# Kernel tuning notes

Measured on AMD Instinct MI355X. Metric: run time of the kernel, lower is better.

Reference implementation:

```python
import jax, jax.numpy as jnp
import numpy as np

N_NODES = 100000
N_EDGES = 1600000
D_IN = 64
D_OUT = 64


def setup_inputs() -> dict:
    key = jax.random.key(0)
    k1, k2, k3, k4 = jax.random.split(key, 4)
    x = jax.random.normal(k1, (N_NODES, D_IN), dtype=jnp.float32)
    edge_index = jax.random.randint(k2, (2, N_EDGES), 0, N_NODES, dtype=jnp.int64)
    W = jax.random.normal(k3, (D_OUT, D_IN), dtype=jnp.float32) * (1.0 / np.sqrt(D_IN))
    b = jax.random.normal(k4, (D_OUT,), dtype=jnp.float32) * 0.01
    return {"x": x, "edge_index": edge_index, "W": W, "b": b}


def reference(x, edge_index, W, b):
    num_nodes = x.shape[0]
    row, col = edge_index[0], edge_index[1]
    # degree of each node as a destination (scatter_add of ones over row)
    deg = jax.ops.segment_sum(jnp.ones(row.shape[0], dtype=x.dtype), row,
                              num_segments=num_nodes)
    # deg^-0.5 with inf (deg==0) replaced by 0
    deg_inv_sqrt = jnp.where(deg > 0, jax.lax.rsqrt(jnp.maximum(deg, 1.0)) * jnp.where(deg > 0, 1.0, 0.0), 0.0)
    deg_inv_sqrt = jnp.where(deg > 0, deg ** -0.5, 0.0)
    # gather source features, scale by source norm, scatter-add to destinations
    weighted = x[col] * deg_inv_sqrt[col][:, None]          # [E, D_IN]
    agg = jax.ops.segment_sum(weighted, row, num_segments=num_nodes)  # [N, D_IN]
    agg = agg * deg_inv_sqrt[:, None]
    # linear + relu (torch Linear: y = agg @ W.T + b)
    return jax.nn.relu(agg @ W.T + b)
```

## Files before the change

### kernel.cpp

```cpp
#include <hip/hip_runtime.h>

#define N_NODES 100000
#define N_EDGES 1600000
#define NE4 400000
#define D 64

#define CSHIFT 7
#define CNODES 128
#define NCB 782
#define CAPC 2560
#define COLBITS 17
#define COLMASK 0x1FFFF

#define EPB 16384
#define SBLKS 98
#define XBLKS 1563

#define CCUR_OFF   0
#define CPAIRS_OFF 3200
#define RS_OFF     8010880
#define DINV_OFF   8412288
#define Y_OFF      8813696

typedef float fvec4 __attribute__((ext_vector_type(4)));
typedef __attribute__((ext_vector_type(8))) short bf16x8;
typedef __attribute__((ext_vector_type(4))) float f32x4;

__device__ __forceinline__ float bf2f(unsigned short u) {
    return __uint_as_float(((unsigned)u) << 16);
}
__device__ __forceinline__ unsigned f2bf(float f) {
    unsigned bits = __float_as_uint(f);
    return (bits + 0x7FFFu + ((bits >> 16) & 1u)) >> 16;
}

__global__ __launch_bounds__(256) void fat_kernel(
        const float* __restrict__ x, const float* __restrict__ W,
        const int* __restrict__ row, const int* __restrict__ col,
        int* __restrict__ ccur, int* __restrict__ cpairs,
        unsigned short* __restrict__ y) {
    __shared__ int lcnt[NCB];
    __shared__ int lbase[NCB];
    int t = threadIdx.x;
    if (blockIdx.x < SBLKS) {
        const int4* r4 = (const int4*)row;
        const int4* c4 = (const int4*)col;
        int base4 = blockIdx.x * (EPB / 4);
        for (int i = t; i < NCB; i += 256) lcnt[i] = 0;
        __syncthreads();
#pragma unroll
        for (int i = 0; i < EPB / 1024; ++i) {
            int i4 = base4 + i * 256 + t;
            if (i4 < NE4) {
                int4 rv = r4[i4];
                atomicAdd(&lcnt[rv.x >> CSHIFT], 1);
                atomicAdd(&lcnt[rv.y >> CSHIFT], 1);
                atomicAdd(&lcnt[rv.z >> CSHIFT], 1);
                atomicAdd(&lcnt[rv.w >> CSHIFT], 1);
            }
        }
        __syncthreads();
        for (int i = t; i < NCB; i += 256) {
            int cc = lcnt[i];
            lbase[i] = cc ? atomicAdd(&ccur[i], cc) : 0;
            lcnt[i] = 0;
        }
        __syncthreads();
#pragma unroll
        for (int i = 0; i < EPB / 1024; ++i) {
            int i4 = base4 + i * 256 + t;
            if (i4 < NE4) {
                int4 rv = r4[i4];
                int4 cv = c4[i4];
                int b0 = rv.x >> CSHIFT, b1 = rv.y >> CSHIFT;
                int b2 = rv.z >> CSHIFT, b3 = rv.w >> CSHIFT;
                int p0 = lbase[b0] + atomicAdd(&lcnt[b0], 1);
                int p1 = lbase[b1] + atomicAdd(&lcnt[b1], 1);
                int p2 = lbase[b2] + atomicAdd(&lcnt[b2], 1);
                int p3 = lbase[b3] + atomicAdd(&lcnt[b3], 1);
                if (p0 < CAPC) cpairs[(size_t)b0 * CAPC + p0] = ((rv.x & (CNODES - 1)) << COLBITS) | cv.x;
                if (p1 < CAPC) cpairs[(size_t)b1 * CAPC + p1] = ((rv.y & (CNODES - 1)) << COLBITS) | cv.y;
                if (p2 < CAPC) cpairs[(size_t)b2 * CAPC + p2] = ((rv.z & (CNODES - 1)) << COLBITS) | cv.z;
                if (p3 < CAPC) cpairs[(size_t)b3 * CAPC + p3] = ((rv.w & (CNODES - 1)) << COLBITS) | cv.w;
            }
        }
        return;
    }
    int wave = t >> 6, lane = t & 63;
    int n0w = (blockIdx.x - SBLKS) * 64 + wave * 16;
    if (n0w >= N_NODES) return;
    int lm = lane & 15;
    int g  = lane >> 4;
    bf16x8 ahi[2], alo[2];
    const float* xr = x + (size_t)(n0w + lm) * D + g * 8;
#pragma unroll
    for (int ks = 0; ks < 2; ++ks) {
        float4 fa = *(const float4*)(xr + ks * 32);
        float4 fb = *(const float4*)(xr + ks * 32 + 4);
        float f[8] = {fa.x, fa.y, fa.z, fa.w, fb.x, fb.y, fb.z, fb.w};
#pragma unroll
        for (int j = 0; j < 8; ++j) {
            unsigned hb = f2bf(f[j]);
            float r = f[j] - bf2f((unsigned short)hb);
            ahi[ks][j] = (short)hb;
            alo[ks][j] = (short)f2bf(r);
        }
    }
#pragma unroll
    for (int jt = 0; jt < 4; ++jt) {
        const float* wr = W + (size_t)(jt * 16 + lm) * D + g * 8;
        bf16x8 whi[2], wlo[2];
#pragma unroll
        for (int ks = 0; ks < 2; ++ks) {
            float4 fa = *(const float4*)(wr + ks * 32);
            float4 fb = *(const float4*)(wr + ks * 32 + 4);
            float f[8] = {fa.x, fa.y, fa.z, fa.w, fb.x, fb.y, fb.z, fb.w};
#pragma unroll
            for (int j = 0; j < 8; ++j) {
                unsigned hb = f2bf(f[j]);
                float r = f[j] - bf2f((unsigned short)hb);
                whi[ks][j] = (short)hb;
                wlo[ks][j] = (short)f2bf(r);
            }
        }
        f32x4 acc = {0.0f, 0.0f, 0.0f, 0.0f};
#pragma unroll
        for (int ks = 0; ks < 2; ++ks) {
            acc = __builtin_amdgcn_mfma_f32_16x16x32_bf16(ahi[ks], whi[ks], acc, 0, 0, 0);
            acc = __builtin_amdgcn_mfma_f32_16x16x32_bf16(alo[ks], whi[ks], acc, 0, 0, 0);
            acc = __builtin_amdgcn_mfma_f32_16x16x32_bf16(ahi[ks], wlo[ks], acc, 0, 0, 0);
        }
#pragma unroll
        for (int r = 0; r < 4; ++r) {
            int n = n0w + g * 4 + r;
            y[(size_t)n * D + jt * 16 + lm] = (unsigned short)f2bf(acc[r]);
        }
    }
}

__global__ __launch_bounds__(256) void hist_kernel(
        const int* __restrict__ ccur, const int* __restrict__ cpairs,
        int* __restrict__ rs, float* __restrict__ dinv) {
    __shared__ int hist[CNODES];
    __shared__ int sc[CNODES];
    int t = threadIdx.x;
    int cb = blockIdx.x;
    int base = cb * CAPC;
    int cnt = ccur[cb]; if (cnt > CAPC) cnt = CAPC;
    if (t < CNODES) hist[t] = 0;
    __syncthreads();
    for (int i = t; i < cnt; i += 256)
        atomicAdd(&hist[cpairs[base + i] >> COLBITS], 1);
    __syncthreads();
    int hv = (t < CNODES) ? hist[t] : 0;
    if (t < CNODES) sc[t] = hv;
    __syncthreads();
    for (int off = 1; off < CNODES; off <<= 1) {
        int u = (t < CNODES && t >= off) ? sc[t - off] : 0;
        __syncthreads();
        if (t < CNODES) sc[t] += u;
        __syncthreads();
    }
    if (t < CNODES) {
        int n = (cb << CSHIFT) + t;
        if (n < N_NODES) {
            rs[n] = base + sc[t] - hv;
            dinv[n] = (hv > 0) ? rsqrtf((float)hv) : 0.0f;
        }
    }
}

__global__ __launch_bounds__(512, 4) void megab_kernel(
        const int* __restrict__ ccur, const int* __restrict__ cpairs,
        const int* __restrict__ rs, const float* __restrict__ dinv,
        const unsigned short* __restrict__ y,
        const float* __restrict__ bias, float* __restrict__ out) {
    __shared__ int scol[CAPC];
    __shared__ int cur[CNODES];
    __shared__ int sst[CNODES + 1];
    int t = threadIdx.x;
    int cb = blockIdx.x;
    int base = cb * CAPC;
    int cnt = ccur[cb]; if (cnt > CAPC) cnt = CAPC;
    if (t < CNODES) {
        int n = (cb << CSHIFT) + t;
        int v = (n < N_NODES) ? rs[n] - base : cnt;
        cur[t] = v;
        sst[t] = v;
    }
    if (t == 0) sst[CNODES] = cnt;
    __syncthreads();
    for (int i = t; i < cnt; i += 512) {
        int p = cpairs[base + i];
        int pos = atomicAdd(&cur[p >> COLBITS], 1);
        scol[pos] = p & COLMASK;
    }
    __syncthreads();
    int wave = t >> 6, lane = t & 63;
    int g = lane >> 3, q = lane & 7;
    float bj[8];
    {
        float4 b0 = *(const float4*)(bias + q * 8);
        float4 b1 = *(const float4*)(bias + q * 8 + 4);
        bj[0] = b0.x; bj[1] = b0.y; bj[2] = b0.z; bj[3] = b0.w;
        bj[4] = b1.x; bj[5] = b1.y; bj[6] = b1.z; bj[7] = b1.w;
    }
#pragma unroll 1
    for (int pass = 0; pass < 2; ++pass) {
        int ln = pass * 64 + wave * 8 + g;
        int n = (cb << CSHIFT) + ln;
        int s = sst[ln], d = sst[ln + 1] - s;
        float a[8];
#pragma unroll
        for (int j = 0; j < 8; ++j) a[j] = 0.0f;
        int c8[8];
#pragma unroll
        for (int u = 0; u < 8; ++u) c8[u] = (u < d) ? scol[s + u] : 0;
        for (int k = 0; k < d; k += 8) {
            uint4 v[8];
            float dv8[8];
#pragma unroll
            for (int u = 0; u < 8; ++u) {
                if (k + u < d) {
                    int c = c8[u];
                    dv8[u] = dinv[c];
                    v[u] = *(const uint4*)(y + (size_t)c * D + q * 8);
                }
            }
#pragma unroll
            for (int u = 0; u < 8; ++u) {
                int e2 = k + 8 + u;
                c8[u] = (e2 < d) ? scol[s + e2] : 0;
            }
#pragma unroll
            for (int u = 0; u < 8; ++u) {
                if (k + u < d) {
                    float dvu = dv8[u];
                    a[0] = fmaf(dvu, __uint_as_float(v[u].x << 16),         a[0]);
                    a[1] = fmaf(dvu, __uint_as_float(v[u].x & 0xffff0000u), a[1]);
                    a[2] = fmaf(dvu, __uint_as_float(v[u].y << 16),         a[2]);
                    a[3] = fmaf(dvu, __uint_as_float(v[u].y & 0xffff0000u), a[3]);
                    a[4] = fmaf(dvu, __uint_as_float(v[u].z << 16),         a[4]);
                    a[5] = fmaf(dvu, __uint_as_float(v[u].z & 0xffff0000u), a[5]);
                    a[6] = fmaf(dvu, __uint_as_float(v[u].w << 16),         a[6]);
                    a[7] = fmaf(dvu, __uint_as_float(v[u].w & 0xffff0000u), a[7]);
                }
            }
        }
        if (n < N_NODES) {
            float dvn = dinv[n];
            fvec4 r0, r1;
            r0.x = fmaxf(fmaf(dvn, a[0], bj[0]), 0.0f);
            r0.y = fmaxf(fmaf(dvn, a[1], bj[1]), 0.0f);
            r0.z = fmaxf(fmaf(dvn, a[2], bj[2]), 0.0f);
            r0.w = fmaxf(fmaf(dvn, a[3], bj[3]), 0.0f);
            r1.x = fmaxf(fmaf(dvn, a[4], bj[4]), 0.0f);
            r1.y = fmaxf(fmaf(dvn, a[5], bj[5]), 0.0f);
            r1.z = fmaxf(fmaf(dvn, a[6], bj[6]), 0.0f);
            r1.w = fmaxf(fmaf(dvn, a[7], bj[7]), 0.0f);
            __builtin_nontemporal_store(r0, (fvec4*)(out + (size_t)n * D + q * 8));
            __builtin_nontemporal_store(r1, (fvec4*)(out + (size_t)n * D + q * 8 + 4));
        }
    }
}

extern "C" void kernel_launch(void* const* d_in, const int* in_sizes, int n_in,
                              void* d_out, int out_size, void* d_ws, size_t ws_size,
                              hipStream_t stream) {
    const float* x    = (const float*)d_in[0];
    const int*   eidx = (const int*)d_in[1];
    const float* W    = (const float*)d_in[2];
    const float* b    = (const float*)d_in[3];
    float* out = (float*)d_out;
    char* ws = (char*)d_ws;

    const int* row = eidx;
    const int* col = eidx + N_EDGES;

    int* ccur   = (int*)(ws + CCUR_OFF);
    int* cpairs = (int*)(ws + CPAIRS_OFF);
    int* rs     = (int*)(ws + RS_OFF);
    float* dinv = (float*)(ws + DINV_OFF);
    unsigned short* y = (unsigned short*)(ws + Y_OFF);

    hipMemsetAsync(ccur, 0, NCB * sizeof(int), stream);
    fat_kernel<<<SBLKS + XBLKS, 256, 0, stream>>>(x, W, row, col, ccur, cpairs, y);
    hist_kernel<<<NCB, 256, 0, stream>>>(ccur, cpairs, rs, dinv);
    megab_kernel<<<NCB, 512, 0, stream>>>(ccur, cpairs, rs, dinv, y, b, out);
}
```

Before: 161.1 us.

## Fuse memset, scatter, hist and gather into one cooperative persistent kernel

```diff
diff --git a/kernel.cpp b/kernel.cpp
--- a/kernel.cpp
+++ b/kernel.cpp
@@ -1,4 +1,7 @@
 #include <hip/hip_runtime.h>
+#include <hip/hip_cooperative_groups.h>
+
+namespace cg = cooperative_groups;
 
 #define N_NODES 100000
 #define N_EDGES 1600000
@@ -12,9 +15,9 @@
 #define COLBITS 17
 #define COLMASK 0x1FFFF
 
-#define EPB 16384
-#define SBLKS 98
-#define XBLKS 1563
+#define EPB 8192
+#define SBLKS 196
+#define GRID 512
 
 #define CCUR_OFF   0
 #define CPAIRS_OFF 3200
@@ -34,65 +37,64 @@
     return (bits + 0x7FFFu + ((bits >> 16) & 1u)) >> 16;
 }
 
-__global__ __launch_bounds__(256) void fat_kernel(
-        const float* __restrict__ x, const float* __restrict__ W,
+
+__device__ __forceinline__ void dev_scatter(int sb, int t,
         const int* __restrict__ row, const int* __restrict__ col,
         int* __restrict__ ccur, int* __restrict__ cpairs,
+        int* lcnt, int* lbase) {
+    const int4* r4 = (const int4*)row;
+    const int4* c4 = (const int4*)col;
+    int base4 = sb * (EPB / 4);
+    for (int i = t; i < NCB; i += 512) lcnt[i] = 0;
+    __syncthreads();
+#pragma unroll
+    for (int i = 0; i < EPB / 2048; ++i) {
+        int i4 = base4 + i * 512 + t;
+        if (i4 < NE4) {
+            int4 rv = r4[i4];
+            atomicAdd(&lcnt[rv.x >> CSHIFT], 1);
+            atomicAdd(&lcnt[rv.y >> CSHIFT], 1);
+            atomicAdd(&lcnt[rv.z >> CSHIFT], 1);
+            atomicAdd(&lcnt[rv.w >> CSHIFT], 1);
+        }
+    }
+    __syncthreads();
+    for (int i = t; i < NCB; i += 512) {
+        int cc = lcnt[i];
+        lbase[i] = cc ? atomicAdd(&ccur[i], cc) : 0;
+        lcnt[i] = 0;
+    }
+    __syncthreads();
+#pragma unroll
+    for (int i = 0; i < EPB / 2048; ++i) {
+        int i4 = base4 + i * 512 + t;
+        if (i4 < NE4) {
+            int4 rv = r4[i4];
+            int4 cv = c4[i4];
+            int b0 = rv.x >> CSHIFT, b1 = rv.y >> CSHIFT;
+            int b2 = rv.z >> CSHIFT, b3 = rv.w >> CSHIFT;
+            int p0 = lbase[b0] + atomicAdd(&lcnt[b0], 1);
+            int p1 = lbase[b1] + atomicAdd(&lcnt[b1], 1);
+            int p2 = lbase[b2] + atomicAdd(&lcnt[b2], 1);
+            int p3 = lbase[b3] + atomicAdd(&lcnt[b3], 1);
+            if (p0 < CAPC) cpairs[(size_t)b0 * CAPC + p0] = ((rv.x & (CNODES - 1)) << COLBITS) | cv.x;
+            if (p1 < CAPC) cpairs[(size_t)b1 * CAPC + p1] = ((rv.y & (CNODES - 1)) << COLBITS) | cv.y;
+            if (p2 < CAPC) cpairs[(size_t)b2 * CAPC + p2] = ((rv.z & (CNODES - 1)) << COLBITS) | cv.z;
+            if (p3 < CAPC) cpairs[(size_t)b3 * CAPC + p3] = ((rv.w & (CNODES - 1)) << COLBITS) | cv.w;
+        }
+    }
+}
+
+__device__ __forceinline__ void dev_xform(int u, int t,
+        const float* __restrict__ x, const float* __restrict__ W,
         unsigned short* __restrict__ y) {
-    __shared__ int lcnt[NCB];
-    __shared__ int lbase[NCB];
-    int t = threadIdx.x;
-    if (blockIdx.x < SBLKS) {
-        const int4* r4 = (const int4*)row;
-        const int4* c4 = (const int4*)col;
-        int base4 = blockIdx.x * (EPB / 4);
-        for (int i = t; i < NCB; i += 256) lcnt[i] = 0;
-        __syncthreads();
-#pragma unroll
-        for (int i = 0; i < EPB / 1024; ++i) {
-            int i4 = base4 + i * 256 + t;
-            if (i4 < NE4) {
-                int4 rv = r4[i4];
-                atomicAdd(&lcnt[rv.x >> CSHIFT], 1);
-                atomicAdd(&lcnt[rv.y >> CSHIFT], 1);
-                atomicAdd(&lcnt[rv.z >> CSHIFT], 1);
-                atomicAdd(&lcnt[rv.w >> CSHIFT], 1);
-            }
-        }
-        __syncthreads();
-        for (int i = t; i < NCB; i += 256) {
-            int cc = lcnt[i];
-            lbase[i] = cc ? atomicAdd(&ccur[i], cc) : 0;
-            lcnt[i] = 0;
-        }
-        __syncthreads();
-#pragma unroll
-        for (int i = 0; i < EPB / 1024; ++i) {
-            int i4 = base4 + i * 256 + t;
-            if (i4 < NE4) {
-                int4 rv = r4[i4];
-                int4 cv = c4[i4];
-                int b0 = rv.x >> CSHIFT, b1 = rv.y >> CSHIFT;
-                int b2 = rv.z >> CSHIFT, b3 = rv.w >> CSHIFT;
-                int p0 = lbase[b0] + atomicAdd(&lcnt[b0], 1);
-                int p1 = lbase[b1] + atomicAdd(&lcnt[b1], 1);
-                int p2 = lbase[b2] + atomicAdd(&lcnt[b2], 1);
-                int p3 = lbase[b3] + atomicAdd(&lcnt[b3], 1);
-                if (p0 < CAPC) cpairs[(size_t)b0 * CAPC + p0] = ((rv.x & (CNODES - 1)) << COLBITS) | cv.x;
-                if (p1 < CAPC) cpairs[(size_t)b1 * CAPC + p1] = ((rv.y & (CNODES - 1)) << COLBITS) | cv.y;
-                if (p2 < CAPC) cpairs[(size_t)b2 * CAPC + p2] = ((rv.z & (CNODES - 1)) << COLBITS) | cv.z;
-                if (p3 < CAPC) cpairs[(size_t)b3 * CAPC + p3] = ((rv.w & (CNODES - 1)) << COLBITS) | cv.w;
-            }
-        }
-        return;
-    }
     int wave = t >> 6, lane = t & 63;
-    int n0w = (blockIdx.x - SBLKS) * 64 + wave * 16;
+    int n0w = u * 128 + wave * 16;
     if (n0w >= N_NODES) return;
     int lm = lane & 15;
-    int g  = lane >> 4;
+    int gg = lane >> 4;
     bf16x8 ahi[2], alo[2];
-    const float* xr = x + (size_t)(n0w + lm) * D + g * 8;
+    const float* xr = x + (size_t)(n0w + lm) * D + gg * 8;
 #pragma unroll
     for (int ks = 0; ks < 2; ++ks) {
         float4 fa = *(const float4*)(xr + ks * 32);
@@ -108,7 +110,7 @@
     }
 #pragma unroll
     for (int jt = 0; jt < 4; ++jt) {
-        const float* wr = W + (size_t)(jt * 16 + lm) * D + g * 8;
+        const float* wr = W + (size_t)(jt * 16 + lm) * D + gg * 8;
         bf16x8 whi[2], wlo[2];
 #pragma unroll
         for (int ks = 0; ks < 2; ++ks) {
@@ -132,24 +134,22 @@
         }
 #pragma unroll
         for (int r = 0; r < 4; ++r) {
-            int n = n0w + g * 4 + r;
+            int n = n0w + gg * 4 + r;
             y[(size_t)n * D + jt * 16 + lm] = (unsigned short)f2bf(acc[r]);
         }
     }
 }
 
-__global__ __launch_bounds__(256) void hist_kernel(
+__device__ __forceinline__ void dev_hist(int b, int t,
         const int* __restrict__ ccur, const int* __restrict__ cpairs,
-        int* __restrict__ rs, float* __restrict__ dinv) {
-    __shared__ int hist[CNODES];
-    __shared__ int sc[CNODES];
-    int t = threadIdx.x;
-    int cb = blockIdx.x;
-    int base = cb * CAPC;
-    int cnt = ccur[cb]; if (cnt > CAPC) cnt = CAPC;
+        int* __restrict__ rs, float* __restrict__ dinv,
+        int* hist, int* sc) {
+    __syncthreads();
+    int base = b * CAPC;
+    int cnt = ccur[b]; if (cnt > CAPC) cnt = CAPC;
     if (t < CNODES) hist[t] = 0;
     __syncthreads();
-    for (int i = t; i < cnt; i += 256)
+    for (int i = t; i < cnt; i += 512)
         atomicAdd(&hist[cpairs[base + i] >> COLBITS], 1);
     __syncthreads();
     int hv = (t < CNODES) ? hist[t] : 0;
@@ -162,7 +162,7 @@
         __syncthreads();
     }
     if (t < CNODES) {
-        int n = (cb << CSHIFT) + t;
+        int n = (b << CSHIFT) + t;
         if (n < N_NODES) {
             rs[n] = base + sc[t] - hv;
             dinv[n] = (hv > 0) ? rsqrtf((float)hv) : 0.0f;
@@ -170,20 +170,17 @@
     }
 }
 
-__global__ __launch_bounds__(512, 4) void megab_kernel(
+__device__ __forceinline__ void dev_gather(int b, int t,
         const int* __restrict__ ccur, const int* __restrict__ cpairs,
         const int* __restrict__ rs, const float* __restrict__ dinv,
         const unsigned short* __restrict__ y,
-        const float* __restrict__ bias, float* __restrict__ out) {
-    __shared__ int scol[CAPC];
-    __shared__ int cur[CNODES];
-    __shared__ int sst[CNODES + 1];
-    int t = threadIdx.x;
-    int cb = blockIdx.x;
-    int base = cb * CAPC;
-    int cnt = ccur[cb]; if (cnt > CAPC) cnt = CAPC;
+        const float* __restrict__ bias, float* __restrict__ out,
+        int* scol, int* cur, int* sst) {
+    __syncthreads();
+    int base = b * CAPC;
+    int cnt = ccur[b]; if (cnt > CAPC) cnt = CAPC;
     if (t < CNODES) {
-        int n = (cb << CSHIFT) + t;
+        int n = (b << CSHIFT) + t;
         int v = (n < N_NODES) ? rs[n] - base : cnt;
         cur[t] = v;
         sst[t] = v;
@@ -208,7 +205,7 @@
 #pragma unroll 1
     for (int pass = 0; pass < 2; ++pass) {
         int ln = pass * 64 + wave * 8 + g;
-        int n = (cb << CSHIFT) + ln;
+        int n = (b << CSHIFT) + ln;
         int s = sst[ln], d = sst[ln + 1] - s;
         float a[8];
 #pragma unroll
@@ -264,13 +261,83 @@
     }
 }
 
+__global__ __launch_bounds__(512, 4) void gcn_kernel(
+        const float* __restrict__ x, const float* __restrict__ W,
+        const int* __restrict__ row, const int* __restrict__ col,
+        int* __restrict__ ccur, int* __restrict__ cpairs,
+        int* __restrict__ rs, float* __restrict__ dinv,
+        unsigned short* __restrict__ y,
+        const float* __restrict__ bias, float* __restrict__ out) {
+    cg::grid_group grid = cg::this_grid();
+    __shared__ int lcnt[NCB];
+    __shared__ int lbase[NCB];
+    __shared__ int hist[CNODES];
+    __shared__ int sc[CNODES];
+    __shared__ int scol[CAPC];
+    __shared__ int cur[CNODES];
+    __shared__ int sst[CNODES + 1];
+    int t = threadIdx.x;
+    int b = blockIdx.x;
+
+    for (int i = b * 512 + t; i < NCB; i += GRID * 512) ccur[i] = 0;
+    grid.sync();
+
+    if (b < SBLKS) {
+        dev_scatter(b, t, row, col, ccur, cpairs, lcnt, lbase);
+    } else {
+        for (int u = b - SBLKS; u < NCB; u += GRID - SBLKS)
+            dev_xform(u, t, x, W, y);
+    }
+    grid.sync();
+
+    for (int bb = b; bb < NCB; bb += GRID)
+        dev_hist(bb, t, ccur, cpairs, rs, dinv, hist, sc);
+    grid.sync();
+
+    for (int bb = b; bb < NCB; bb += GRID)
+        dev_gather(bb, t, ccur, cpairs, rs, dinv, y, bias, out, scol, cur, sst);
+}
+
+__global__ __launch_bounds__(512, 4) void fb_fat_kernel(
+        const float* __restrict__ x, const float* __restrict__ W,
+        const int* __restrict__ row, const int* __restrict__ col,
+        int* __restrict__ ccur, int* __restrict__ cpairs,
+        unsigned short* __restrict__ y) {
+    __shared__ int lcnt[NCB];
+    __shared__ int lbase[NCB];
+    if (blockIdx.x < SBLKS)
+        dev_scatter(blockIdx.x, threadIdx.x, row, col, ccur, cpairs, lcnt, lbase);
+    else
+        dev_xform(blockIdx.x - SBLKS, threadIdx.x, x, W, y);
+}
+
+__global__ __launch_bounds__(512, 4) void fb_hist_kernel(
+        const int* __restrict__ ccur, const int* __restrict__ cpairs,
+        int* __restrict__ rs, float* __restrict__ dinv) {
+    __shared__ int hist[CNODES];
+    __shared__ int sc[CNODES];
+    dev_hist(blockIdx.x, threadIdx.x, ccur, cpairs, rs, dinv, hist, sc);
+}
+
+__global__ __launch_bounds__(512, 4) void fb_gath_kernel(
+        const int* __restrict__ ccur, const int* __restrict__ cpairs,
+        const int* __restrict__ rs, const float* __restrict__ dinv,
+        const unsigned short* __restrict__ y,
+        const float* __restrict__ bias, float* __restrict__ out) {
+    __shared__ int scol[CAPC];
+    __shared__ int cur[CNODES];
+    __shared__ int sst[CNODES + 1];
+    dev_gather(blockIdx.x, threadIdx.x, ccur, cpairs, rs, dinv, y, bias, out,
+               scol, cur, sst);
+}
+
 extern "C" void kernel_launch(void* const* d_in, const int* in_sizes, int n_in,
                               void* d_out, int out_size, void* d_ws, size_t ws_size,
                               hipStream_t stream) {
     const float* x    = (const float*)d_in[0];
     const int*   eidx = (const int*)d_in[1];
     const float* W    = (const float*)d_in[2];
-    const float* b    = (const float*)d_in[3];
+    const float* bias = (const float*)d_in[3];
     float* out = (float*)d_out;
     char* ws = (char*)d_ws;
 
@@ -283,8 +350,15 @@
     float* dinv = (float*)(ws + DINV_OFF);
     unsigned short* y = (unsigned short*)(ws + Y_OFF);
 
-    hipMemsetAsync(ccur, 0, NCB * sizeof(int), stream);
-    fat_kernel<<<SBLKS + XBLKS, 256, 0, stream>>>(x, W, row, col, ccur, cpairs, y);
-    hist_kernel<<<NCB, 256, 0, stream>>>(ccur, cpairs, rs, dinv);
-    megab_kernel<<<NCB, 512, 0, stream>>>(ccur, cpairs, rs, dinv, y, b, out);
-}
+    void* args[] = {(void*)&x, (void*)&W, (void*)&row, (void*)&col,
+                    (void*)&ccur, (void*)&cpairs, (void*)&rs, (void*)&dinv,
+                    (void*)&y, (void*)&bias, (void*)&out};
+    hipError_t err = hipLaunchCooperativeKernel((void*)gcn_kernel, dim3(GRID),
+                                                dim3(512), args, 0, stream);
+    if (err != hipSuccess) {
+        hipMemsetAsync(ccur, 0, NCB * sizeof(int), stream);
+        fb_fat_kernel<<<SBLKS + NCB, 512, 0, stream>>>(x, W, row, col, ccur, cpairs, y);
+        fb_hist_kernel<<<NCB, 512, 0, stream>>>(ccur, cpairs, rs, dinv);
+        fb_gath_kernel<<<NCB, 512, 0, stream>>>(ccur, cpairs, rs, dinv, y, bias, out);
+    }
+}
```

Result: slower. 311.6 us (+93.5%).

## Replace global atomic bucketing with per-block fixed segments and drop counter memset

Applied to the files above, without the earlier changes.

```diff
diff --git a/kernel.cpp b/kernel.cpp
--- a/kernel.cpp
+++ b/kernel.cpp
@@ -14,13 +14,15 @@
 
 #define EPB 16384
 #define SBLKS 98
-#define XBLKS 1563
-
-#define CCUR_OFF   0
-#define CPAIRS_OFF 3200
-#define RS_OFF     8010880
-#define DINV_OFF   8412288
-#define Y_OFF      8813696
+#define SEGSHIFT 6
+#define SEGI 64
+#define SEGP 63
+#define XUNITS 782
+
+#define CP_OFF    0
+#define RS_OFF    19619840
+#define DINV_OFF  20021248
+#define Y_OFF     20422656
 
 typedef float fvec4 __attribute__((ext_vector_type(4)));
 typedef __attribute__((ext_vector_type(8))) short bf16x8;
@@ -34,65 +36,56 @@
     return (bits + 0x7FFFu + ((bits >> 16) & 1u)) >> 16;
 }
 
-__global__ __launch_bounds__(256) void fat_kernel(
+__global__ __launch_bounds__(512, 4) void fat_kernel(
         const float* __restrict__ x, const float* __restrict__ W,
         const int* __restrict__ row, const int* __restrict__ col,
-        int* __restrict__ ccur, int* __restrict__ cpairs,
-        unsigned short* __restrict__ y) {
+        int* __restrict__ cpairs, unsigned short* __restrict__ y) {
     __shared__ int lcnt[NCB];
-    __shared__ int lbase[NCB];
     int t = threadIdx.x;
     if (blockIdx.x < SBLKS) {
+        int k = blockIdx.x;
         const int4* r4 = (const int4*)row;
         const int4* c4 = (const int4*)col;
-        int base4 = blockIdx.x * (EPB / 4);
-        for (int i = t; i < NCB; i += 256) lcnt[i] = 0;
-        __syncthreads();
-#pragma unroll
-        for (int i = 0; i < EPB / 1024; ++i) {
-            int i4 = base4 + i * 256 + t;
-            if (i4 < NE4) {
-                int4 rv = r4[i4];
-                atomicAdd(&lcnt[rv.x >> CSHIFT], 1);
-                atomicAdd(&lcnt[rv.y >> CSHIFT], 1);
-                atomicAdd(&lcnt[rv.z >> CSHIFT], 1);
-                atomicAdd(&lcnt[rv.w >> CSHIFT], 1);
-            }
-        }
-        __syncthreads();
-        for (int i = t; i < NCB; i += 256) {
-            int cc = lcnt[i];
-            lbase[i] = cc ? atomicAdd(&ccur[i], cc) : 0;
-            lcnt[i] = 0;
-        }
-        __syncthreads();
-#pragma unroll
-        for (int i = 0; i < EPB / 1024; ++i) {
-            int i4 = base4 + i * 256 + t;
+        int base4 = k * (EPB / 4);
+        for (int i = t; i < NCB; i += 512) lcnt[i] = 0;
+        __syncthreads();
+#pragma unroll
+        for (int i = 0; i < EPB / 2048; ++i) {
+            int i4 = base4 + i * 512 + t;
             if (i4 < NE4) {
                 int4 rv = r4[i4];
                 int4 cv = c4[i4];
                 int b0 = rv.x >> CSHIFT, b1 = rv.y >> CSHIFT;
                 int b2 = rv.z >> CSHIFT, b3 = rv.w >> CSHIFT;
-                int p0 = lbase[b0] + atomicAdd(&lcnt[b0], 1);
-                int p1 = lbase[b1] + atomicAdd(&lcnt[b1], 1);
-                int p2 = lbase[b2] + atomicAdd(&lcnt[b2], 1);
-                int p3 = lbase[b3] + atomicAdd(&lcnt[b3], 1);
-                if (p0 < CAPC) cpairs[(size_t)b0 * CAPC + p0] = ((rv.x & (CNODES - 1)) << COLBITS) | cv.x;
-                if (p1 < CAPC) cpairs[(size_t)b1 * CAPC + p1] = ((rv.y & (CNODES - 1)) << COLBITS) | cv.y;
-                if (p2 < CAPC) cpairs[(size_t)b2 * CAPC + p2] = ((rv.z & (CNODES - 1)) << COLBITS) | cv.z;
-                if (p3 < CAPC) cpairs[(size_t)b3 * CAPC + p3] = ((rv.w & (CNODES - 1)) << COLBITS) | cv.w;
-            }
+                int p0 = atomicAdd(&lcnt[b0], 1);
+                int p1 = atomicAdd(&lcnt[b1], 1);
+                int p2 = atomicAdd(&lcnt[b2], 1);
+                int p3 = atomicAdd(&lcnt[b3], 1);
+                if (p0 < SEGP) cpairs[((b0 * SBLKS + k) << SEGSHIFT) + 1 + p0] =
+                    ((rv.x & (CNODES - 1)) << COLBITS) | cv.x;
+                if (p1 < SEGP) cpairs[((b1 * SBLKS + k) << SEGSHIFT) + 1 + p1] =
+                    ((rv.y & (CNODES - 1)) << COLBITS) | cv.y;
+                if (p2 < SEGP) cpairs[((b2 * SBLKS + k) << SEGSHIFT) + 1 + p2] =
+                    ((rv.z & (CNODES - 1)) << COLBITS) | cv.z;
+                if (p3 < SEGP) cpairs[((b3 * SBLKS + k) << SEGSHIFT) + 1 + p3] =
+                    ((rv.w & (CNODES - 1)) << COLBITS) | cv.w;
+            }
+        }
+        __syncthreads();
+        for (int b = t; b < NCB; b += 512) {
+            int c = lcnt[b]; if (c > SEGP) c = SEGP;
+            cpairs[(b * SBLKS + k) << SEGSHIFT] = c;
         }
         return;
     }
     int wave = t >> 6, lane = t & 63;
-    int n0w = (blockIdx.x - SBLKS) * 64 + wave * 16;
+    int u = blockIdx.x - SBLKS;
+    int n0w = u * 128 + wave * 16;
     if (n0w >= N_NODES) return;
     int lm = lane & 15;
-    int g  = lane >> 4;
+    int gg = lane >> 4;
     bf16x8 ahi[2], alo[2];
-    const float* xr = x + (size_t)(n0w + lm) * D + g * 8;
+    const float* xr = x + (size_t)(n0w + lm) * D + gg * 8;
 #pragma unroll
     for (int ks = 0; ks < 2; ++ks) {
         float4 fa = *(const float4*)(xr + ks * 32);
@@ -108,7 +101,7 @@
     }
 #pragma unroll
     for (int jt = 0; jt < 4; ++jt) {
-        const float* wr = W + (size_t)(jt * 16 + lm) * D + g * 8;
+        const float* wr = W + (size_t)(jt * 16 + lm) * D + gg * 8;
         bf16x8 whi[2], wlo[2];
 #pragma unroll
         for (int ks = 0; ks < 2; ++ks) {
@@ -132,25 +125,30 @@
         }
 #pragma unroll
         for (int r = 0; r < 4; ++r) {
-            int n = n0w + g * 4 + r;
+            int n = n0w + gg * 4 + r;
             y[(size_t)n * D + jt * 16 + lm] = (unsigned short)f2bf(acc[r]);
         }
     }
 }
 
 __global__ __launch_bounds__(256) void hist_kernel(
-        const int* __restrict__ ccur, const int* __restrict__ cpairs,
+        const int* __restrict__ cpairs,
         int* __restrict__ rs, float* __restrict__ dinv) {
+    __shared__ int cntk[SBLKS];
     __shared__ int hist[CNODES];
     __shared__ int sc[CNODES];
     int t = threadIdx.x;
-    int cb = blockIdx.x;
-    int base = cb * CAPC;
-    int cnt = ccur[cb]; if (cnt > CAPC) cnt = CAPC;
+    int b = blockIdx.x;
+    int rbase = (b * SBLKS) << SEGSHIFT;
+    if (t < SBLKS) cntk[t] = cpairs[rbase + (t << SEGSHIFT)];
     if (t < CNODES) hist[t] = 0;
     __syncthreads();
-    for (int i = t; i < cnt; i += 256)
-        atomicAdd(&hist[cpairs[base + i] >> COLBITS], 1);
+    for (int i = t; i < SBLKS * SEGI; i += 256) {
+        int j = i & (SEGI - 1);
+        int k = i >> SEGSHIFT;
+        if (j >= 1 && j <= cntk[k])
+            atomicAdd(&hist[cpairs[rbase + i] >> COLBITS], 1);
+    }
     __syncthreads();
     int hv = (t < CNODES) ? hist[t] : 0;
     if (t < CNODES) sc[t] = hv;
@@ -162,38 +160,48 @@
         __syncthreads();
     }
     if (t < CNODES) {
-        int n = (cb << CSHIFT) + t;
+        int n = (b << CSHIFT) + t;
         if (n < N_NODES) {
-            rs[n] = base + sc[t] - hv;
+            rs[n] = sc[t] - hv;
             dinv[n] = (hv > 0) ? rsqrtf((float)hv) : 0.0f;
         }
     }
 }
 
-__global__ __launch_bounds__(512, 4) void megab_kernel(
-        const int* __restrict__ ccur, const int* __restrict__ cpairs,
-        const int* __restrict__ rs, const float* __restrict__ dinv,
-        const unsigned short* __restrict__ y,
+__global__ __launch_bounds__(256) void gath_kernel(
+        const int* __restrict__ cpairs, const int* __restrict__ rs,
+        const float* __restrict__ dinv, const unsigned short* __restrict__ y,
         const float* __restrict__ bias, float* __restrict__ out) {
+    __shared__ int cntk[SBLKS];
     __shared__ int scol[CAPC];
     __shared__ int cur[CNODES];
     __shared__ int sst[CNODES + 1];
+    __shared__ int tot;
     int t = threadIdx.x;
-    int cb = blockIdx.x;
-    int base = cb * CAPC;
-    int cnt = ccur[cb]; if (cnt > CAPC) cnt = CAPC;
+    int b = blockIdx.x;
+    int rbase = (b * SBLKS) << SEGSHIFT;
+    if (t < SBLKS) cntk[t] = cpairs[rbase + (t << SEGSHIFT)];
+    if (t == 0) tot = 0;
+    __syncthreads();
+    if (t < SBLKS) atomicAdd(&tot, cntk[t]);
+    __syncthreads();
+    int cnt = tot; if (cnt > CAPC) cnt = CAPC;
     if (t < CNODES) {
-        int n = (cb << CSHIFT) + t;
-        int v = (n < N_NODES) ? rs[n] - base : cnt;
+        int n = (b << CSHIFT) + t;
+        int v = (n < N_NODES) ? rs[n] : cnt;
         cur[t] = v;
         sst[t] = v;
     }
     if (t == 0) sst[CNODES] = cnt;
     __syncthreads();
-    for (int i = t; i < cnt; i += 512) {
-        int p = cpairs[base + i];
-        int pos = atomicAdd(&cur[p >> COLBITS], 1);
-        scol[pos] = p & COLMASK;
+    for (int i = t; i < SBLKS * SEGI; i += 256) {
+        int j = i & (SEGI - 1);
+        int k = i >> SEGSHIFT;
+        if (j >= 1 && j <= cntk[k]) {
+            int p = cpairs[rbase + i];
+            int pos = atomicAdd(&cur[p >> COLBITS], 1);
+            if (pos < CAPC) scol[pos] = p & COLMASK;
+        }
     }
     __syncthreads();
     int wave = t >> 6, lane = t & 63;
@@ -206,9 +214,9 @@
         bj[4] = b1.x; bj[5] = b1.y; bj[6] = b1.z; bj[7] = b1.w;
     }
 #pragma unroll 1
-    for (int pass = 0; pass < 2; ++pass) {
-        int ln = pass * 64 + wave * 8 + g;
-        int n = (cb << CSHIFT) + ln;
+    for (int pass = 0; pass < 4; ++pass) {
+        int ln = pass * 32 + wave * 8 + g;
+        int n = (b << CSHIFT) + ln;
         int s = sst[ln], d = sst[ln + 1] - s;
         float a[8];
 #pragma unroll
@@ -270,21 +278,19 @@
     const float* x    = (const float*)d_in[0];
     const int*   eidx = (const int*)d_in[1];
     const float* W    = (const float*)d_in[2];
-    const float* b    = (const float*)d_in[3];
+    const float* bias = (const float*)d_in[3];
     float* out = (float*)d_out;
     char* ws = (char*)d_ws;
 
     const int* row = eidx;
     const int* col = eidx + N_EDGES;
 
-    int* ccur   = (int*)(ws + CCUR_OFF);
-    int* cpairs = (int*)(ws + CPAIRS_OFF);
+    int* cpairs = (int*)(ws + CP_OFF);
     int* rs     = (int*)(ws + RS_OFF);
     float* dinv = (float*)(ws + DINV_OFF);
     unsigned short* y = (unsigned short*)(ws + Y_OFF);
 
-    hipMemsetAsync(ccur, 0, NCB * sizeof(int), stream);
-    fat_kernel<<<SBLKS + XBLKS, 256, 0, stream>>>(x, W, row, col, ccur, cpairs, y);
-    hist_kernel<<<NCB, 256, 0, stream>>>(ccur, cpairs, rs, dinv);
-    megab_kernel<<<NCB, 512, 0, stream>>>(ccur, cpairs, rs, dinv, y, b, out);
-}
+    fat_kernel<<<SBLKS + XUNITS, 512, 0, stream>>>(x, W, row, col, cpairs, y);
+    hist_kernel<<<NCB, 256, 0, stream>>>(cpairs, rs, dinv);
+    gath_kernel<<<NCB, 256, 0, stream>>>(cpairs, rs, dinv, y, bias, out);
+}
```

New measurement: 162.4 us. About the same (+0.8%).
